# Performance work log

Hardware: AMD Instinct MI355X
Metric: run time of the kernel (lower is better)

Reference implementation:

```python
import jax, jax.numpy as jnp
import numpy as np
from math import sqrt

B, S, D_MODEL, H, DK, DV = 16, 512, 256, 8, 32, 32
EPS = 1e-5


def layer_norm(x, g, b):
    m = jnp.mean(x, axis=-1, keepdims=True)
    v = jnp.mean((x - m) ** 2, axis=-1, keepdims=True)
    return g * (x - m) / jnp.sqrt(v + EPS) + b


def setup_inputs() -> dict:
    key = jax.random.key(0)
    ks = jax.random.split(key, 16)
    inp = {
        "input_Q": jax.random.normal(ks[0], (B, S, D_MODEL), jnp.float32),
        "input_K": jax.random.normal(ks[1], (B, S, D_MODEL), jnp.float32),
        "input_V": jax.random.normal(ks[2], (B, S, D_MODEL), jnp.float32),
        "attn_mask": jax.random.bernoulli(ks[3], 0.1, (B, H, S, S)),
        "matrix": jax.random.uniform(ks[4], (B, S, S), jnp.float32),
        # learned params (stored [in, out], i.e. transpose of torch Linear weight)
        "W_Q": jax.random.normal(ks[5], (D_MODEL, H * DK), jnp.float32) * 0.02,
        "W_K": jax.random.normal(ks[6], (D_MODEL, H * DK), jnp.float32) * 0.02,
        "W_V": jax.random.normal(ks[7], (D_MODEL, H * DV), jnp.float32) * 0.02,
        "W_V2": jax.random.normal(ks[8], (D_MODEL, DV), jnp.float32) * 0.02,
        "W_fc": jax.random.normal(ks[9], (DV * (H + 1), D_MODEL), jnp.float32) * 0.02,
        "ln_g": jnp.ones((D_MODEL,), jnp.float32),
        "ln_b": jnp.zeros((D_MODEL,), jnp.float32),
        "fu_ln_g": jnp.ones((H + 1,), jnp.float32),
        "fu_ln_b": jnp.zeros((H + 1,), jnp.float32),
        "fu_w1": jax.random.normal(ks[10], (H + 1, 6), jnp.float32) * 0.3,
        "fu_b1": jnp.zeros((6,), jnp.float32),
        "fu_w2": jax.random.normal(ks[11], (6, 1), jnp.float32) * 0.3,
        "fu_b2": jnp.zeros((1,), jnp.float32),
    }
    return inp


def reference(input_Q, input_K, input_V, attn_mask, matrix,
              W_Q, W_K, W_V, W_V2, W_fc, ln_g, ln_b,
              fu_ln_g, fu_ln_b, fu_w1, fu_b1, fu_w2, fu_b2):
    b = input_Q.shape[0]
    # project and split heads: [B, H, S, d]
    Q = (input_Q @ W_Q).reshape(b, -1, H, DK).transpose(0, 2, 1, 3)
    K = (input_K @ W_K).reshape(b, -1, H, DK).transpose(0, 2, 1, 3)
    V = (input_V @ W_V).reshape(b, -1, H, DV).transpose(0, 2, 1, 3)
    scores = jnp.einsum('bhqd,bhkd->bhqk', Q, K) / sqrt(DK)
    scores = jnp.where(attn_mask, -1e9, scores)
    attn = jax.nn.softmax(scores, axis=-1)            # [B, H, S, S]
    context = jnp.einsum('bhqk,bhkd->bhqd', attn, V)  # [B, H, S, DV]
    # second context from pairwise matrix
    context2 = matrix @ (input_V @ W_V2)              # [B, S, DV]
    # gated matrix update: concat matrix with attn maps along head axis
    gate_in = jnp.concatenate([matrix[:, None], attn], axis=1)  # [B, H+1, S, S]
    gate_in = gate_in.transpose(0, 3, 2, 1)                     # [B, S, S, H+1]
    g = layer_norm(gate_in, fu_ln_g, fu_ln_b)
    g = jax.nn.relu(g @ fu_w1 + fu_b1)
    g = jax.nn.sigmoid(g @ fu_w2 + fu_b2)[..., 0]               # [B, S, S]
    matrix_out = matrix * g
    # merge heads, concat, project, layernorm
    context = context.transpose(0, 2, 1, 3).reshape(b, -1, H * DV)
    context = jnp.concatenate([context, context2], axis=-1)     # [B, S, DV*(H+1)]
    output = layer_norm(context @ W_fc, ln_g, ln_b)
    return (output, matrix_out)
```

## Files before the change

### kernel.cpp

```cpp
#include <hip/hip_runtime.h>
#include <hip/hip_bf16.h>

#define BB 16
#define SS 512
#define DM 256
#define NH 8

#define OFF_QB    0
#define OFF_KB    1048576
#define OFF_VT    2097152
#define OFF_VP2   3145728
#define OFF_CTXB  3407872
#define OFF_CTX2B 4456448
#define OFF_G     4587520
#define OFF_FLAG  6684672
#define OFF_PM    6684674

#define SCALE 0.17677669529663687f
#define KE2 0.2550348623f

typedef __attribute__((ext_vector_type(8))) short bfrag8;
typedef __attribute__((ext_vector_type(4))) float facc4;

__global__ void mask_or_kernel(const unsigned int* __restrict__ w,
                               unsigned int* __restrict__ acc) {
  __shared__ unsigned int sh[256];
  unsigned int a = 0;
  int base = blockIdx.x * 1024;
  for (int i = threadIdx.x; i < 1024; i += 256) a |= w[base + i];
  sh[threadIdx.x] = a;
  __syncthreads();
  for (int s = 128; s > 0; s >>= 1) {
    if (threadIdx.x < s) sh[threadIdx.x] |= sh[threadIdx.x + s];
    __syncthreads();
  }
  if (threadIdx.x == 0) atomicOr(acc, sh[0]);
}

__global__ __launch_bounds__(256) void mask_pack_kernel(
    const void* __restrict__ mask, unsigned long long* __restrict__ pm,
    const unsigned int* __restrict__ orv) {
  const unsigned int rawor = *orv;
  const int flagv = (rawor <= 1u) ? 0 : ((rawor == 0x3F800000u) ? 2 : 1);
  const int lane = threadIdx.x & 63;
  const int wv = threadIdx.x >> 6;
  const int w0 = (blockIdx.x * 4 + wv) * 32;
  const unsigned char* mb = (const unsigned char*)mask;
  const int* mi = (const int*)mask;
  const float* mf = (const float*)mask;
  unsigned long long myw = 0;
#pragma unroll 4
  for (int i = 0; i < 32; i++) {
    long long idx = (long long)(w0 + i) * 64 + lane;
    bool m;
    if (flagv == 1) m = (mb[idx] != 0);
    else if (flagv == 0) m = (mi[idx] != 0);
    else m = (mf[idx] != 0.f);
    unsigned long long bits = __ballot(m);
    if (lane == i) myw = bits;
  }
  if (lane < 32) pm[w0 + lane] = myw;
}

__global__ __launch_bounds__(256) void gemm_qkv_kernel(
    const float* __restrict__ inQ, const float* __restrict__ inK,
    const float* __restrict__ inV,
    const float* __restrict__ Wq, const float* __restrict__ Wk,
    const float* __restrict__ Wv,
    __hip_bfloat16* __restrict__ Qb, __hip_bfloat16* __restrict__ Kb,
    __hip_bfloat16* __restrict__ Vt) {
  __shared__ __align__(16) __hip_bfloat16 As[64][40];
  __shared__ __align__(16) __hip_bfloat16 Bs[64][40];
  const int tid = threadIdx.x;
  const int bid = blockIdx.x;
  const int matid = bid >> 9;
  const int mblk = (bid & 511) >> 2;
  const int nblk = bid & 3;
  const int m0 = mblk * 64;
  const int n0 = nblk * 64;
  const float* X = (matid == 0) ? inQ : (matid == 1) ? inK : inV;
  const float* W = (matid == 0) ? Wq : (matid == 1) ? Wk : Wv;

  const int lane = tid & 63;
  const int w = tid >> 6;
  const int wm = w & 1, wn = w >> 1;
  const int cl = lane & 15, quad = lane >> 4;
  const int arow = tid >> 2, ak8 = (tid & 3) * 8;
  const int bn = tid & 63, bk8 = (tid >> 6) * 8;

  facc4 acc[2][2];
#pragma unroll
  for (int t = 0; t < 2; t++)
#pragma unroll
    for (int u = 0; u < 2; u++) acc[t][u] = (facc4){0.f, 0.f, 0.f, 0.f};

#pragma unroll 1
  for (int kc = 0; kc < 8; kc++) {
    float4 x0 = *(const float4*)&X[(m0 + arow) * 256 + kc * 32 + ak8];
    float4 x1 = *(const float4*)&X[(m0 + arow) * 256 + kc * 32 + ak8 + 4];
    float wv[8];
#pragma unroll
    for (int j = 0; j < 8; j++) wv[j] = W[(kc * 32 + bk8 + j) * 256 + n0 + bn];
    __syncthreads();
    {
      __hip_bfloat16 ta[8];
      ta[0] = __float2bfloat16(x0.x); ta[1] = __float2bfloat16(x0.y);
      ta[2] = __float2bfloat16(x0.z); ta[3] = __float2bfloat16(x0.w);
      ta[4] = __float2bfloat16(x1.x); ta[5] = __float2bfloat16(x1.y);
      ta[6] = __float2bfloat16(x1.z); ta[7] = __float2bfloat16(x1.w);
      *(uint4*)&As[arow][ak8] = *(uint4*)ta;
      __hip_bfloat16 tb[8];
#pragma unroll
      for (int j = 0; j < 8; j++) tb[j] = __float2bfloat16(wv[j]);
      *(uint4*)&Bs[bn][bk8] = *(uint4*)tb;
    }
    __syncthreads();
    bfrag8 aA[2], bB[2];
#pragma unroll
    for (int t = 0; t < 2; t++)
      aA[t] = *(const bfrag8*)&As[wm * 32 + t * 16 + cl][quad * 8];
#pragma unroll
    for (int u = 0; u < 2; u++)
      bB[u] = *(const bfrag8*)&Bs[wn * 32 + u * 16 + cl][quad * 8];
#pragma unroll
    for (int t = 0; t < 2; t++)
#pragma unroll
      for (int u = 0; u < 2; u++)
        acc[t][u] =
            __builtin_amdgcn_mfma_f32_16x16x32_bf16(aA[t], bB[u], acc[t][u], 0, 0, 0);
  }

  if (matid < 2) {
    __hip_bfloat16* Y = (matid == 0) ? Qb : Kb;
#pragma unroll
    for (int t = 0; t < 2; t++)
#pragma unroll
      for (int u = 0; u < 2; u++)
#pragma unroll
        for (int reg = 0; reg < 4; reg++)
          Y[(m0 + wm * 32 + t * 16 + quad * 4 + reg) * 256 + n0 + wn * 32 +
            u * 16 + cl] = __float2bfloat16(acc[t][u][reg]);
  } else {
#pragma unroll
    for (int t = 0; t < 2; t++)
#pragma unroll
      for (int u = 0; u < 2; u++) {
        int c = n0 + wn * 32 + u * 16 + cl;
        int mg = m0 + wm * 32 + t * 16 + quad * 4;
        int b = mg >> 9, s = mg & 511;
        __hip_bfloat16 pk[4];
#pragma unroll
        for (int reg = 0; reg < 4; reg++)
          pk[reg] = __float2bfloat16(acc[t][u][reg]);
        *(ushort4*)&Vt[(((b << 8) + c) << 9) + s] = *(ushort4*)pk;
      }
  }
}

__global__ __launch_bounds__(256) void vp2_kernel(
    const float* __restrict__ inV, const float* __restrict__ Wv2,
    float* __restrict__ Vp2) {
  __shared__ __align__(16) float xs[16][260];
  const int t = threadIdx.x;
  const int r0 = blockIdx.x * 16;
  for (int e = t; e < 16 * 256; e += 256) {
    int r = e >> 8, i = e & 255;
    xs[r][i] = inV[(r0 + r) * 256 + i];
  }
  __syncthreads();
  const int c2 = t & 31, rr = t >> 5;
  float a0 = 0.f, a1 = 0.f;
  for (int i = 0; i < 256; i += 4) {
    float w0 = Wv2[i * 32 + c2], w1 = Wv2[(i + 1) * 32 + c2];
    float w2 = Wv2[(i + 2) * 32 + c2], w3 = Wv2[(i + 3) * 32 + c2];
    float4 xa = *(const float4*)&xs[rr][i];
    float4 xb = *(const float4*)&xs[rr + 8][i];
    a0 += xa.x * w0 + xa.y * w1 + xa.z * w2 + xa.w * w3;
    a1 += xb.x * w0 + xb.y * w1 + xb.z * w2 + xb.w * w3;
  }
  Vp2[(r0 + rr) * 32 + c2] = a0;
  Vp2[(r0 + rr + 8) * 32 + c2] = a1;
}

__global__ __launch_bounds__(512, 2) void attn_kernel(
    const __hip_bfloat16* __restrict__ Qb, const __hip_bfloat16* __restrict__ Kb,
    const __hip_bfloat16* __restrict__ Vt,
    const unsigned long long* __restrict__ pm,
    const float* __restrict__ matrix,
    const float* __restrict__ fulng, const float* __restrict__ fulnb,
    const float* __restrict__ fuw1, const float* __restrict__ fub1,
    const float* __restrict__ fuw2, const float* __restrict__ fub2,
    __hip_bfloat16* __restrict__ ctxb, __hip_bfloat16* __restrict__ gws) {
  __shared__ __align__(16) __hip_bfloat16 Sb[NH][16][520];
  __shared__ float inv_s[NH][16];
  __shared__ float gp[80];

  const int tid = threadIdx.x;
  const int lane = tid & 63;
  const int h = tid >> 6;
  const int cl = lane & 15, quad = lane >> 4;
  const int b = ((blockIdx.x & 7) << 1) | (blockIdx.x >> 8);
  const int q0 = ((blockIdx.x >> 3) & 31) * 16;

  if (tid < 6) {
    const int j = tid;
    float s1 = 0.f, c1 = fub1[j];
#pragma unroll
    for (int t = 0; t < 9; t++) {
      float w = fuw1[t * 6 + j];
      float gw = fulng[t] * w;
      gp[t * 6 + j] = gw;
      s1 += gw;
      c1 += fulnb[t] * w;
    }
    gp[54 + j] = s1;
    gp[60 + j] = c1;
    gp[66 + j] = fuw2[j];
    if (j == 0) gp[72] = fub2[0];
  }

  const unsigned long long* pmb = pm + (((b * NH + h) << 9) + q0) * 8;

  const bfrag8 aQ =
      *(const bfrag8*)&Qb[(((b << 9) + q0 + cl) << 8) + h * 32 + quad * 8];
  const __hip_bfloat16* KbB = &Kb[((b << 9) << 8) + h * 32 + quad * 8];
  const __hip_bfloat16* VtB = &Vt[(((b << 8) + h * 32) << 9)];

  float l[4] = {0.f, 0.f, 0.f, 0.f};
#pragma unroll 4
  for (int w8 = 0; w8 < 8; w8++) {
    unsigned long long mw[4];
#pragma unroll
    for (int r = 0; r < 4; r++)
      mw[r] = pmb[(quad * 4 + r) * 8 + w8] >> cl;
#pragma unroll
    for (int n4 = 0; n4 < 4; n4++) {
      const int nt = w8 * 4 + n4;
      bfrag8 bK = *(const bfrag8*)&KbB[(nt * 16 + cl) << 8];
      facc4 cc = {0.f, 0.f, 0.f, 0.f};
      cc = __builtin_amdgcn_mfma_f32_16x16x32_bf16(aQ, bK, cc, 0, 0, 0);
#pragma unroll
      for (int r = 0; r < 4; r++) {
        float e = ((mw[r] >> (n4 * 16)) & 1ULL) ? 0.f : exp2f(KE2 * cc[r]);
        l[r] += e;
        Sb[h][quad * 4 + r][nt * 16 + cl] = __float2bfloat16(e);
      }
    }
  }
#pragma unroll
  for (int r = 0; r < 4; r++)
#pragma unroll
    for (int off = 1; off <= 8; off <<= 1) l[r] += __shfl_xor(l[r], off);
  float invl[4];
#pragma unroll
  for (int r = 0; r < 4; r++) invl[r] = 1.f / l[r];
  if (cl == 0) {
#pragma unroll
    for (int r = 0; r < 4; r++) inv_s[h][quad * 4 + r] = invl[r];
  }
  __syncthreads();

  facc4 a0 = {0.f, 0.f, 0.f, 0.f}, a1 = {0.f, 0.f, 0.f, 0.f};
#pragma unroll 8
  for (int ks = 0; ks < 16; ks++) {
    bfrag8 aP = *(const bfrag8*)&Sb[h][cl][ks * 32 + quad * 8];
    bfrag8 b0 = *(const bfrag8*)&VtB[(cl << 9) + ks * 32 + quad * 8];
    bfrag8 b1 = *(const bfrag8*)&VtB[((16 + cl) << 9) + ks * 32 + quad * 8];
    a0 = __builtin_amdgcn_mfma_f32_16x16x32_bf16(aP, b0, a0, 0, 0, 0);
    a1 = __builtin_amdgcn_mfma_f32_16x16x32_bf16(aP, b1, a1, 0, 0, 0);
  }

  {
    const int gq = tid >> 5;
    const int g32 = (tid & 31) * 4;
#pragma unroll 2
    for (int s = 0; s < 4; s++) {
      const int k4 = s * 128 + g32;
      float4 mrow =
          *(const float4*)&matrix[((b << 9) + q0 + gq) * 512 + k4];
      float p[NH][4];
#pragma unroll
      for (int hh = 0; hh < NH; hh++) {
        const float iv = inv_s[hh][gq];
        ushort4 sv = *(const ushort4*)&Sb[hh][gq][k4];
        p[hh][0] = __bfloat162float(*(__hip_bfloat16*)&sv.x) * iv;
        p[hh][1] = __bfloat162float(*(__hip_bfloat16*)&sv.y) * iv;
        p[hh][2] = __bfloat162float(*(__hip_bfloat16*)&sv.z) * iv;
        p[hh][3] = __bfloat162float(*(__hip_bfloat16*)&sv.w) * iv;
      }
      const float mcomp[4] = {mrow.x, mrow.y, mrow.z, mrow.w};
      __hip_bfloat16 gout[4];
#pragma unroll
      for (int i = 0; i < 4; i++) {
        float v[9];
        v[0] = mcomp[i];
#pragma unroll
        for (int t = 0; t < NH; t++) v[1 + t] = p[t][i];
        float s1 = 0.f, s2 = 0.f;
#pragma unroll
        for (int t = 0; t < 9; t++) {
          s1 += v[t];
          s2 += v[t] * v[t];
        }
        float mu = s1 * (1.f / 9.f);
        float var = s2 * (1.f / 9.f) - mu * mu;
        float inv = rsqrtf(var + 1e-5f);
        float o = gp[72];
#pragma unroll
        for (int j = 0; j < 6; j++) {
          float d = 0.f;
#pragma unroll
          for (int t = 0; t < 9; t++) d += v[t] * gp[t * 6 + j];
          float z = inv * (d - mu * gp[54 + j]) + gp[60 + j];
          z = fmaxf(z, 0.f);
          o += z * gp[66 + j];
        }
        gout[i] = __float2bfloat16(1.f / (1.f + __expf(-o)));
      }
      *(ushort4*)&gws[((b << 9) + q0 + gq) * 512 + k4] = *(ushort4*)gout;
    }
  }

#pragma unroll
  for (int r = 0; r < 4; r++) {
    int row = quad * 4 + r;
    ctxb[((b << 9) + q0 + row) * 256 + h * 32 + cl] =
        __float2bfloat16(a0[r] * invl[r]);
    ctxb[((b << 9) + q0 + row) * 256 + h * 32 + 16 + cl] =
        __float2bfloat16(a1[r] * invl[r]);
  }
}

__global__ __launch_bounds__(256) void mout_kernel(
    const float* __restrict__ matrix, const __hip_bfloat16* __restrict__ g,
    float* __restrict__ mout) {
  __shared__ float Gs[64][65];
  const int tid = threadIdx.x;
  const int b = blockIdx.x >> 6;
  const int j0 = ((blockIdx.x >> 3) & 7) * 64;
  const int i0 = (blockIdx.x & 7) * 64;

  {
    int r = tid >> 2, c0 = (tid & 3) * 16;
    const __hip_bfloat16* gpx = g + (((b << 9) + i0 + r) << 9) + j0 + c0;
    ushort us[16];
    *(uint4*)(us) = *(const uint4*)(gpx);
    *(uint4*)(us + 8) = *(const uint4*)(gpx + 8);
#pragma unroll
    for (int k = 0; k < 16; k++) {
      __hip_bfloat16 hv = *(__hip_bfloat16*)&us[k];
      Gs[r][c0 + k] = __bfloat162float(hv);
    }
  }
  __syncthreads();

  {
    int jj = tid >> 2, ic = (tid & 3) * 16;
    const float* mp = matrix + (((b << 9) + j0 + jj) << 9) + i0 + ic;
    float* op = mout + (((b << 9) + j0 + jj) << 9) + i0 + ic;
#pragma unroll
    for (int v4 = 0; v4 < 4; v4++) {
      float4 m = *(const float4*)(mp + v4 * 4);
      float4 o;
      o.x = m.x * Gs[ic + v4 * 4 + 0][jj];
      o.y = m.y * Gs[ic + v4 * 4 + 1][jj];
      o.z = m.z * Gs[ic + v4 * 4 + 2][jj];
      o.w = m.w * Gs[ic + v4 * 4 + 3][jj];
      *(float4*)(op + v4 * 4) = o;
    }
  }
}

__global__ __launch_bounds__(256) void ctx2_kernel(
    const float* __restrict__ matrix, const float* __restrict__ Vp2,
    __hip_bfloat16* __restrict__ ctx2b) {
  __shared__ __align__(16) float Ms[16][128];
  __shared__ __align__(16) float Vs2t[32][132];
  const int t = threadIdx.x;
  const int b = blockIdx.x >> 5;
  const int s0 = (blockIdx.x & 31) * 16;
  const int dv = t & 31, rg = t >> 5;
  float acc0 = 0.f, acc1 = 0.f;
  for (int kc = 0; kc < 4; kc++) {
    __syncthreads();
#pragma unroll
    for (int it = 0; it < 8; it++) {
      int idx = t + it * 256;
      int r = idx >> 7, cc = idx & 127;
      Ms[r][cc] = matrix[((b << 9) + s0 + r) * 512 + kc * 128 + cc];
    }
#pragma unroll
    for (int it = 0; it < 16; it++) {
      int e = t + it * 256;
      int k = e >> 5, dv2 = e & 31;
      Vs2t[dv2][k] = Vp2[((b << 9) + kc * 128 + k) * 32 + dv2];
    }
    __syncthreads();
    for (int k = 0; k < 128; k += 4) {
      float4 vv = *(const float4*)&Vs2t[dv][k];
      float4 m0 = *(const float4*)&Ms[rg][k];
      float4 m1 = *(const float4*)&Ms[rg + 8][k];
      acc0 += m0.x * vv.x + m0.y * vv.y + m0.z * vv.z + m0.w * vv.w;
      acc1 += m1.x * vv.x + m1.y * vv.y + m1.z * vv.z + m1.w * vv.w;
    }
  }
  ctx2b[((b << 9) + s0 + rg) * 32 + dv] = __float2bfloat16(acc0);
  ctx2b[((b << 9) + s0 + rg + 8) * 32 + dv] = __float2bfloat16(acc1);
}

__global__ __launch_bounds__(256) void final_kernel(
    const __hip_bfloat16* __restrict__ ctxb,
    const __hip_bfloat16* __restrict__ ctx2b, const float* __restrict__ Wfc,
    const float* __restrict__ lng, const float* __restrict__ lnb,
    float* __restrict__ out) {
  __shared__ __align__(16) __hip_bfloat16 As[32][40];
  __shared__ __align__(16) __hip_bfloat16 Bs[256][40];
  __shared__ __align__(16) float xs[32][260];
  __shared__ float red2[32][8][2];
  __shared__ float musig[32][2];
  const int tid = threadIdx.x;
  const int m0 = blockIdx.x * 32;
  const int lane = tid & 63, w = tid >> 6;
  const int cl = lane & 15, quad = lane >> 4;
  const int arow = tid >> 3, ak4 = (tid & 7) * 4;

  facc4 acc[2][4];
#pragma unroll
  for (int t = 0; t < 2; t++)
#pragma unroll
    for (int u = 0; u < 4; u++) acc[t][u] = (facc4){0.f, 0.f, 0.f, 0.f};

#pragma unroll 1
  for (int kc = 0; kc < 9; kc++) {
    ushort4 av;
    if (kc < 8)
      av = *(const ushort4*)&ctxb[(m0 + arow) * 256 + kc * 32 + ak4];
    else
      av = *(const ushort4*)&ctx2b[(m0 + arow) * 32 + ak4];
    float wv[32];
#pragma unroll
    for (int j = 0; j < 32; j++) wv[j] = Wfc[(kc * 32 + j) * 256 + tid];
    __syncthreads();
    *(ushort4*)&As[arow][ak4] = av;
    {
      __hip_bfloat16 tw[32];
#pragma unroll
      for (int j = 0; j < 32; j++) tw[j] = __float2bfloat16(wv[j]);
#pragma unroll
      for (int g = 0; g < 4; g++) *(uint4*)&Bs[tid][g * 8] = *(uint4*)&tw[g * 8];
    }
    __syncthreads();
    bfrag8 aA[2], bB[4];
#pragma unroll
    for (int t = 0; t < 2; t++)
      aA[t] = *(const bfrag8*)&As[t * 16 + cl][quad * 8];
#pragma unroll
    for (int u = 0; u < 4; u++)
      bB[u] = *(const bfrag8*)&Bs[w * 64 + u * 16 + cl][quad * 8];
#pragma unroll
    for (int t = 0; t < 2; t++)
#pragma unroll
      for (int u = 0; u < 4; u++)
        acc[t][u] =
            __builtin_amdgcn_mfma_f32_16x16x32_bf16(aA[t], bB[u], acc[t][u], 0, 0, 0);
  }

#pragma unroll
  for (int t = 0; t < 2; t++)
#pragma unroll
    for (int u = 0; u < 4; u++)
#pragma unroll
      for (int reg = 0; reg < 4; reg++)
        xs[t * 16 + quad * 4 + reg][w * 64 + u * 16 + cl] = acc[t][u][reg];
  __syncthreads();

  {
    int r = tid >> 3, c0 = (tid & 7) * 32;
    float s1 = 0.f, s2 = 0.f;
    for (int j = 0; j < 32; j += 4) {
      float4 v = *(const float4*)&xs[r][c0 + j];
      s1 += v.x + v.y + v.z + v.w;
      s2 += v.x * v.x + v.y * v.y + v.z * v.z + v.w * v.w;
    }
    red2[r][tid & 7][0] = s1;
    red2[r][tid & 7][1] = s2;
  }
  __syncthreads();
  if (tid < 32) {
    float s1 = 0.f, s2 = 0.f;
#pragma unroll
    for (int j = 0; j < 8; j++) {
      s1 += red2[tid][j][0];
      s2 += red2[tid][j][1];
    }
    float mu = s1 * (1.f / 256.f);
    float var = s2 * (1.f / 256.f) - mu * mu;
    musig[tid][0] = mu;
    musig[tid][1] = rsqrtf(var + 1e-5f);
  }
  __syncthreads();
  {
    float gt = lng[tid], bt = lnb[tid];
#pragma unroll 4
    for (int r = 0; r < 32; r++)
      out[(m0 + r) * 256 + tid] =
          gt * (xs[r][tid] - musig[r][0]) * musig[r][1] + bt;
  }
}

extern "C" void kernel_launch(void* const* d_in, const int* in_sizes, int n_in,
                              void* d_out, int out_size, void* d_ws,
                              size_t ws_size, hipStream_t stream) {
  const float* inQ = (const float*)d_in[0];
  const float* inK = (const float*)d_in[1];
  const float* inV = (const float*)d_in[2];
  const void* mask = d_in[3];
  const float* matrix = (const float*)d_in[4];
  const float* Wq = (const float*)d_in[5];
  const float* Wk = (const float*)d_in[6];
  const float* Wv = (const float*)d_in[7];
  const float* Wv2 = (const float*)d_in[8];
  const float* Wfc = (const float*)d_in[9];
  const float* lng = (const float*)d_in[10];
  const float* lnb = (const float*)d_in[11];
  const float* fulng = (const float*)d_in[12];
  const float* fulnb = (const float*)d_in[13];
  const float* fuw1 = (const float*)d_in[14];
  const float* fub1 = (const float*)d_in[15];
  const float* fuw2 = (const float*)d_in[16];
  const float* fub2 = (const float*)d_in[17];

  float* ws = (float*)d_ws;
  __hip_bfloat16* Qb = (__hip_bfloat16*)(ws + OFF_QB);
  __hip_bfloat16* Kb = (__hip_bfloat16*)(ws + OFF_KB);
  __hip_bfloat16* Vt = (__hip_bfloat16*)(ws + OFF_VT);
  float* Vp2 = ws + OFF_VP2;
  __hip_bfloat16* ctxb = (__hip_bfloat16*)(ws + OFF_CTXB);
  __hip_bfloat16* ctx2b = (__hip_bfloat16*)(ws + OFF_CTX2B);
  __hip_bfloat16* gws = (__hip_bfloat16*)(ws + OFF_G);
  unsigned int* flag = (unsigned int*)(ws + OFF_FLAG);
  unsigned long long* pmask = (unsigned long long*)(ws + OFF_PM);

  float* out = (float*)d_out;
  float* mout = out + BB * SS * DM;

  hipMemsetAsync(flag, 0, 4, stream);
  mask_or_kernel<<<64, 256, 0, stream>>>((const unsigned int*)mask, flag);
  mask_pack_kernel<<<4096, 256, 0, stream>>>(mask, pmask, flag);
  gemm_qkv_kernel<<<1536, 256, 0, stream>>>(inQ, inK, inV, Wq, Wk, Wv, Qb, Kb,
                                            Vt);
  vp2_kernel<<<512, 256, 0, stream>>>(inV, Wv2, Vp2);
  attn_kernel<<<512, 512, 0, stream>>>(Qb, Kb, Vt, pmask, matrix, fulng, fulnb,
                                       fuw1, fub1, fuw2, fub2, ctxb, gws);
  mout_kernel<<<BB * 64, 256, 0, stream>>>(matrix, gws, mout);
  ctx2_kernel<<<512, 256, 0, stream>>>(matrix, Vp2, ctx2b);
  final_kernel<<<256, 256, 0, stream>>>(ctxb, ctx2b, Wfc, lng, lnb, out);
}
```

Measured before the change: 396.2 us.

## Merge independent kernels and pick mask packing path from input byte size

Merges the QKV projection GEMM with the V2 projection, and the matrix-gating output with the context2 matmul, into single launches that dispatch on block index. When the mask buffer is 4 bytes per element, the memset and flag-detection kernel are skipped and a dedicated 32-bit packing kernel runs instead. Unroll factors in the attention kernel loops are also reduced, likely to ease register pressure. This cuts launch count and lets independent work share the GPU, at the cost of heterogeneous blocks inside one grid.

```diff
diff --git a/kernel.cpp b/kernel.cpp
--- a/kernel.cpp
+++ b/kernel.cpp
@@ -62,124 +62,139 @@
   if (lane < 32) pm[w0 + lane] = myw;
 }
 
-__global__ __launch_bounds__(256) void gemm_qkv_kernel(
+__global__ __launch_bounds__(256) void mask_pack4_kernel(
+    const unsigned int* __restrict__ mask, unsigned long long* __restrict__ pm) {
+  const int lane = threadIdx.x & 63;
+  const int wv = threadIdx.x >> 6;
+  const int w0 = (blockIdx.x * 4 + wv) * 32;
+  unsigned long long myw = 0;
+#pragma unroll 4
+  for (int i = 0; i < 32; i++) {
+    unsigned int v = mask[(long long)(w0 + i) * 64 + lane];
+    unsigned long long bits = __ballot(v != 0u);
+    if (lane == i) myw = bits;
+  }
+  if (lane < 32) pm[w0 + lane] = myw;
+}
+
+__global__ __launch_bounds__(256) void gemm_qkv_vp2_kernel(
     const float* __restrict__ inQ, const float* __restrict__ inK,
     const float* __restrict__ inV,
     const float* __restrict__ Wq, const float* __restrict__ Wk,
-    const float* __restrict__ Wv,
+    const float* __restrict__ Wv, const float* __restrict__ Wv2,
     __hip_bfloat16* __restrict__ Qb, __hip_bfloat16* __restrict__ Kb,
-    __hip_bfloat16* __restrict__ Vt) {
-  __shared__ __align__(16) __hip_bfloat16 As[64][40];
-  __shared__ __align__(16) __hip_bfloat16 Bs[64][40];
+    __hip_bfloat16* __restrict__ Vt, float* __restrict__ Vp2) {
+  __shared__ __align__(16) char smem[16640];
   const int tid = threadIdx.x;
-  const int bid = blockIdx.x;
-  const int matid = bid >> 9;
-  const int mblk = (bid & 511) >> 2;
-  const int nblk = bid & 3;
-  const int m0 = mblk * 64;
-  const int n0 = nblk * 64;
-  const float* X = (matid == 0) ? inQ : (matid == 1) ? inK : inV;
-  const float* W = (matid == 0) ? Wq : (matid == 1) ? Wk : Wv;
-
-  const int lane = tid & 63;
-  const int w = tid >> 6;
-  const int wm = w & 1, wn = w >> 1;
-  const int cl = lane & 15, quad = lane >> 4;
-  const int arow = tid >> 2, ak8 = (tid & 3) * 8;
-  const int bn = tid & 63, bk8 = (tid >> 6) * 8;
-
-  facc4 acc[2][2];
-#pragma unroll
-  for (int t = 0; t < 2; t++)
-#pragma unroll
-    for (int u = 0; u < 2; u++) acc[t][u] = (facc4){0.f, 0.f, 0.f, 0.f};
+
+  if (blockIdx.x < 1536) {
+    auto As = reinterpret_cast<__hip_bfloat16(*)[40]>(smem);
+    auto Bs = reinterpret_cast<__hip_bfloat16(*)[40]>(smem + 5120);
+    const int bid = blockIdx.x;
+    const int matid = bid >> 9;
+    const int mblk = (bid & 511) >> 2;
+    const int nblk = bid & 3;
+    const int m0 = mblk * 64;
+    const int n0 = nblk * 64;
+    const float* X = (matid == 0) ? inQ : (matid == 1) ? inK : inV;
+    const float* W = (matid == 0) ? Wq : (matid == 1) ? Wk : Wv;
+
+    const int lane = tid & 63;
+    const int w = tid >> 6;
+    const int wm = w & 1, wn = w >> 1;
+    const int cl = lane & 15, quad = lane >> 4;
+    const int arow = tid >> 2, ak8 = (tid & 3) * 8;
+    const int bn = tid & 63, bk8 = (tid >> 6) * 8;
+
+    facc4 acc[2][2];
+#pragma unroll
+    for (int t = 0; t < 2; t++)
+#pragma unroll
+      for (int u = 0; u < 2; u++) acc[t][u] = (facc4){0.f, 0.f, 0.f, 0.f};
 
 #pragma unroll 1
-  for (int kc = 0; kc < 8; kc++) {
-    float4 x0 = *(const float4*)&X[(m0 + arow) * 256 + kc * 32 + ak8];
-    float4 x1 = *(const float4*)&X[(m0 + arow) * 256 + kc * 32 + ak8 + 4];
-    float wv[8];
-#pragma unroll
-    for (int j = 0; j < 8; j++) wv[j] = W[(kc * 32 + bk8 + j) * 256 + n0 + bn];
+    for (int kc = 0; kc < 8; kc++) {
+      float4 x0 = *(const float4*)&X[(m0 + arow) * 256 + kc * 32 + ak8];
+      float4 x1 = *(const float4*)&X[(m0 + arow) * 256 + kc * 32 + ak8 + 4];
+      float wv[8];
+#pragma unroll
+      for (int j = 0; j < 8; j++)
+        wv[j] = W[(kc * 32 + bk8 + j) * 256 + n0 + bn];
+      __syncthreads();
+      {
+        __hip_bfloat16 ta[8];
+        ta[0] = __float2bfloat16(x0.x); ta[1] = __float2bfloat16(x0.y);
+        ta[2] = __float2bfloat16(x0.z); ta[3] = __float2bfloat16(x0.w);
+        ta[4] = __float2bfloat16(x1.x); ta[5] = __float2bfloat16(x1.y);
+        ta[6] = __float2bfloat16(x1.z); ta[7] = __float2bfloat16(x1.w);
+        *(uint4*)&As[arow][ak8] = *(uint4*)ta;
+        __hip_bfloat16 tb[8];
+#pragma unroll
+        for (int j = 0; j < 8; j++) tb[j] = __float2bfloat16(wv[j]);
+        *(uint4*)&Bs[bn][bk8] = *(uint4*)tb;
+      }
+      __syncthreads();
+      bfrag8 aA[2], bB[2];
+#pragma unroll
+      for (int t = 0; t < 2; t++)
+        aA[t] = *(const bfrag8*)&As[wm * 32 + t * 16 + cl][quad * 8];
+#pragma unroll
+      for (int u = 0; u < 2; u++)
+        bB[u] = *(const bfrag8*)&Bs[wn * 32 + u * 16 + cl][quad * 8];
+#pragma unroll
+      for (int t = 0; t < 2; t++)
+#pragma unroll
+        for (int u = 0; u < 2; u++)
+          acc[t][u] = __builtin_amdgcn_mfma_f32_16x16x32_bf16(aA[t], bB[u],
+                                                             acc[t][u], 0, 0, 0);
+    }
+
+    if (matid < 2) {
+      __hip_bfloat16* Y = (matid == 0) ? Qb : Kb;
+#pragma unroll
+      for (int t = 0; t < 2; t++)
+#pragma unroll
+        for (int u = 0; u < 2; u++)
+#pragma unroll
+          for (int reg = 0; reg < 4; reg++)
+            Y[(m0 + wm * 32 + t * 16 + quad * 4 + reg) * 256 + n0 + wn * 32 +
+              u * 16 + cl] = __float2bfloat16(acc[t][u][reg]);
+    } else {
+#pragma unroll
+      for (int t = 0; t < 2; t++)
+#pragma unroll
+        for (int u = 0; u < 2; u++) {
+          int c = n0 + wn * 32 + u * 16 + cl;
+          int mg = m0 + wm * 32 + t * 16 + quad * 4;
+          int b = mg >> 9, s = mg & 511;
+          __hip_bfloat16 pk[4];
+#pragma unroll
+          for (int reg = 0; reg < 4; reg++)
+            pk[reg] = __float2bfloat16(acc[t][u][reg]);
+          *(ushort4*)&Vt[(((b << 8) + c) << 9) + s] = *(ushort4*)pk;
+        }
+    }
+  } else {
+    auto xs = reinterpret_cast<float(*)[260]>(smem);
+    const int r0 = (blockIdx.x - 1536) * 16;
+    for (int e = tid; e < 16 * 256; e += 256) {
+      int r = e >> 8, i = e & 255;
+      xs[r][i] = inV[(r0 + r) * 256 + i];
+    }
     __syncthreads();
-    {
-      __hip_bfloat16 ta[8];
-      ta[0] = __float2bfloat16(x0.x); ta[1] = __float2bfloat16(x0.y);
-      ta[2] = __float2bfloat16(x0.z); ta[3] = __float2bfloat16(x0.w);
-      ta[4] = __float2bfloat16(x1.x); ta[5] = __float2bfloat16(x1.y);
-      ta[6] = __float2bfloat16(x1.z); ta[7] = __float2bfloat16(x1.w);
-      *(uint4*)&As[arow][ak8] = *(uint4*)ta;
-      __hip_bfloat16 tb[8];
-#pragma unroll
-      for (int j = 0; j < 8; j++) tb[j] = __float2bfloat16(wv[j]);
-      *(uint4*)&Bs[bn][bk8] = *(uint4*)tb;
-    }
-    __syncthreads();
-    bfrag8 aA[2], bB[2];
-#pragma unroll
-    for (int t = 0; t < 2; t++)
-      aA[t] = *(const bfrag8*)&As[wm * 32 + t * 16 + cl][quad * 8];
-#pragma unroll
-    for (int u = 0; u < 2; u++)
-      bB[u] = *(const bfrag8*)&Bs[wn * 32 + u * 16 + cl][quad * 8];
-#pragma unroll
-    for (int t = 0; t < 2; t++)
-#pragma unroll
-      for (int u = 0; u < 2; u++)
-        acc[t][u] =
-            __builtin_amdgcn_mfma_f32_16x16x32_bf16(aA[t], bB[u], acc[t][u], 0, 0, 0);
-  }
-
-  if (matid < 2) {
-    __hip_bfloat16* Y = (matid == 0) ? Qb : Kb;
-#pragma unroll
-    for (int t = 0; t < 2; t++)
-#pragma unroll
-      for (int u = 0; u < 2; u++)
-#pragma unroll
-        for (int reg = 0; reg < 4; reg++)
-          Y[(m0 + wm * 32 + t * 16 + quad * 4 + reg) * 256 + n0 + wn * 32 +
-            u * 16 + cl] = __float2bfloat16(acc[t][u][reg]);
-  } else {
-#pragma unroll
-    for (int t = 0; t < 2; t++)
-#pragma unroll
-      for (int u = 0; u < 2; u++) {
-        int c = n0 + wn * 32 + u * 16 + cl;
-        int mg = m0 + wm * 32 + t * 16 + quad * 4;
-        int b = mg >> 9, s = mg & 511;
-        __hip_bfloat16 pk[4];
-#pragma unroll
-        for (int reg = 0; reg < 4; reg++)
-          pk[reg] = __float2bfloat16(acc[t][u][reg]);
-        *(ushort4*)&Vt[(((b << 8) + c) << 9) + s] = *(ushort4*)pk;
-      }
-  }
-}
-
-__global__ __launch_bounds__(256) void vp2_kernel(
-    const float* __restrict__ inV, const float* __restrict__ Wv2,
-    float* __restrict__ Vp2) {
-  __shared__ __align__(16) float xs[16][260];
-  const int t = threadIdx.x;
-  const int r0 = blockIdx.x * 16;
-  for (int e = t; e < 16 * 256; e += 256) {
-    int r = e >> 8, i = e & 255;
-    xs[r][i] = inV[(r0 + r) * 256 + i];
-  }
-  __syncthreads();
-  const int c2 = t & 31, rr = t >> 5;
-  float a0 = 0.f, a1 = 0.f;
-  for (int i = 0; i < 256; i += 4) {
-    float w0 = Wv2[i * 32 + c2], w1 = Wv2[(i + 1) * 32 + c2];
-    float w2 = Wv2[(i + 2) * 32 + c2], w3 = Wv2[(i + 3) * 32 + c2];
-    float4 xa = *(const float4*)&xs[rr][i];
-    float4 xb = *(const float4*)&xs[rr + 8][i];
-    a0 += xa.x * w0 + xa.y * w1 + xa.z * w2 + xa.w * w3;
-    a1 += xb.x * w0 + xb.y * w1 + xb.z * w2 + xb.w * w3;
-  }
-  Vp2[(r0 + rr) * 32 + c2] = a0;
-  Vp2[(r0 + rr + 8) * 32 + c2] = a1;
+    const int c2 = tid & 31, rr = tid >> 5;
+    float a0 = 0.f, a1 = 0.f;
+    for (int i = 0; i < 256; i += 4) {
+      float w0 = Wv2[i * 32 + c2], w1 = Wv2[(i + 1) * 32 + c2];
+      float w2 = Wv2[(i + 2) * 32 + c2], w3 = Wv2[(i + 3) * 32 + c2];
+      float4 xa = *(const float4*)&xs[rr][i];
+      float4 xb = *(const float4*)&xs[rr + 8][i];
+      a0 += xa.x * w0 + xa.y * w1 + xa.z * w2 + xa.w * w3;
+      a1 += xb.x * w0 + xb.y * w1 + xb.z * w2 + xb.w * w3;
+    }
+    Vp2[(r0 + rr) * 32 + c2] = a0;
+    Vp2[(r0 + rr + 8) * 32 + c2] = a1;
+  }
 }
 
 __global__ __launch_bounds__(512, 2) void attn_kernel(
@@ -227,7 +242,7 @@
   const __hip_bfloat16* VtB = &Vt[(((b << 8) + h * 32) << 9)];
 
   float l[4] = {0.f, 0.f, 0.f, 0.f};
-#pragma unroll 4
+#pragma unroll 2
   for (int w8 = 0; w8 < 8; w8++) {
     unsigned long long mw[4];
 #pragma unroll
@@ -261,7 +276,7 @@
   __syncthreads();
 
   facc4 a0 = {0.f, 0.f, 0.f, 0.f}, a1 = {0.f, 0.f, 0.f, 0.f};
-#pragma unroll 8
+#pragma unroll 4
   for (int ks = 0; ks < 16; ks++) {
     bfrag8 aP = *(const bfrag8*)&Sb[h][cl][ks * 32 + quad * 8];
     bfrag8 b0 = *(const bfrag8*)&VtB[(cl << 9) + ks * 32 + quad * 8];
@@ -273,7 +288,7 @@
   {
     const int gq = tid >> 5;
     const int g32 = (tid & 31) * 4;
-#pragma unroll 2
+#pragma unroll 1
     for (int s = 0; s < 4; s++) {
       const int k4 = s * 128 + g32;
       float4 mrow =
@@ -331,81 +346,82 @@
   }
 }
 
-__global__ __launch_bounds__(256) void mout_kernel(
+__global__ __launch_bounds__(256) void mout_ctx2_kernel(
     const float* __restrict__ matrix, const __hip_bfloat16* __restrict__ g,
-    float* __restrict__ mout) {
-  __shared__ float Gs[64][65];
+    float* __restrict__ mout, const float* __restrict__ Vp2,
+    __hip_bfloat16* __restrict__ ctx2b) {
+  __shared__ __align__(16) char smem[25088];
   const int tid = threadIdx.x;
-  const int b = blockIdx.x >> 6;
-  const int j0 = ((blockIdx.x >> 3) & 7) * 64;
-  const int i0 = (blockIdx.x & 7) * 64;
-
-  {
-    int r = tid >> 2, c0 = (tid & 3) * 16;
-    const __hip_bfloat16* gpx = g + (((b << 9) + i0 + r) << 9) + j0 + c0;
-    ushort us[16];
-    *(uint4*)(us) = *(const uint4*)(gpx);
-    *(uint4*)(us + 8) = *(const uint4*)(gpx + 8);
-#pragma unroll
-    for (int k = 0; k < 16; k++) {
-      __hip_bfloat16 hv = *(__hip_bfloat16*)&us[k];
-      Gs[r][c0 + k] = __bfloat162float(hv);
-    }
-  }
-  __syncthreads();
-
-  {
-    int jj = tid >> 2, ic = (tid & 3) * 16;
-    const float* mp = matrix + (((b << 9) + j0 + jj) << 9) + i0 + ic;
-    float* op = mout + (((b << 9) + j0 + jj) << 9) + i0 + ic;
-#pragma unroll
-    for (int v4 = 0; v4 < 4; v4++) {
-      float4 m = *(const float4*)(mp + v4 * 4);
-      float4 o;
-      o.x = m.x * Gs[ic + v4 * 4 + 0][jj];
-      o.y = m.y * Gs[ic + v4 * 4 + 1][jj];
-      o.z = m.z * Gs[ic + v4 * 4 + 2][jj];
-      o.w = m.w * Gs[ic + v4 * 4 + 3][jj];
-      *(float4*)(op + v4 * 4) = o;
-    }
-  }
-}
-
-__global__ __launch_bounds__(256) void ctx2_kernel(
-    const float* __restrict__ matrix, const float* __restrict__ Vp2,
-    __hip_bfloat16* __restrict__ ctx2b) {
-  __shared__ __align__(16) float Ms[16][128];
-  __shared__ __align__(16) float Vs2t[32][132];
-  const int t = threadIdx.x;
-  const int b = blockIdx.x >> 5;
-  const int s0 = (blockIdx.x & 31) * 16;
-  const int dv = t & 31, rg = t >> 5;
-  float acc0 = 0.f, acc1 = 0.f;
-  for (int kc = 0; kc < 4; kc++) {
+
+  if (blockIdx.x < 1024) {
+    auto Gs = reinterpret_cast<float(*)[65]>(smem);
+    const int b = blockIdx.x >> 6;
+    const int j0 = ((blockIdx.x >> 3) & 7) * 64;
+    const int i0 = (blockIdx.x & 7) * 64;
+
+    {
+      int r = tid >> 2, c0 = (tid & 3) * 16;
+      const __hip_bfloat16* gpx = g + (((b << 9) + i0 + r) << 9) + j0 + c0;
+      ushort us[16];
+      *(uint4*)(us) = *(const uint4*)(gpx);
+      *(uint4*)(us + 8) = *(const uint4*)(gpx + 8);
+#pragma unroll
+      for (int k = 0; k < 16; k++) {
+        __hip_bfloat16 hv = *(__hip_bfloat16*)&us[k];
+        Gs[r][c0 + k] = __bfloat162float(hv);
+      }
+    }
     __syncthreads();
-#pragma unroll
-    for (int it = 0; it < 8; it++) {
-      int idx = t + it * 256;
-      int r = idx >> 7, cc = idx & 127;
-      Ms[r][cc] = matrix[((b << 9) + s0 + r) * 512 + kc * 128 + cc];
-    }
-#pragma unroll
-    for (int it = 0; it < 16; it++) {
-      int e = t + it * 256;
-      int k = e >> 5, dv2 = e & 31;
-      Vs2t[dv2][k] = Vp2[((b << 9) + kc * 128 + k) * 32 + dv2];
-    }
-    __syncthreads();
-    for (int k = 0; k < 128; k += 4) {
-      float4 vv = *(const float4*)&Vs2t[dv][k];
-      float4 m0 = *(const float4*)&Ms[rg][k];
-      float4 m1 = *(const float4*)&Ms[rg + 8][k];
-      acc0 += m0.x * vv.x + m0.y * vv.y + m0.z * vv.z + m0.w * vv.w;
-      acc1 += m1.x * vv.x + m1.y * vv.y + m1.z * vv.z + m1.w * vv.w;
-    }
-  }
-  ctx2b[((b << 9) + s0 + rg) * 32 + dv] = __float2bfloat16(acc0);
-  ctx2b[((b << 9) + s0 + rg + 8) * 32 + dv] = __float2bfloat16(acc1);
+
+    {
+      int jj = tid >> 2, ic = (tid & 3) * 16;
+      const float* mp = matrix + (((b << 9) + j0 + jj) << 9) + i0 + ic;
+      float* op = mout + (((b << 9) + j0 + jj) << 9) + i0 + ic;
+#pragma unroll
+      for (int v4 = 0; v4 < 4; v4++) {
+        float4 m = *(const float4*)(mp + v4 * 4);
+        float4 o;
+        o.x = m.x * Gs[ic + v4 * 4 + 0][jj];
+        o.y = m.y * Gs[ic + v4 * 4 + 1][jj];
+        o.z = m.z * Gs[ic + v4 * 4 + 2][jj];
+        o.w = m.w * Gs[ic + v4 * 4 + 3][jj];
+        *(float4*)(op + v4 * 4) = o;
+      }
+    }
+  } else {
+    auto Ms = reinterpret_cast<float(*)[128]>(smem);
+    auto Vs2t = reinterpret_cast<float(*)[132]>(smem + 8192);
+    const int cid = blockIdx.x - 1024;
+    const int b = cid >> 5;
+    const int s0 = (cid & 31) * 16;
+    const int dv = tid & 31, rg = tid >> 5;
+    float acc0 = 0.f, acc1 = 0.f;
+    for (int kc = 0; kc < 4; kc++) {
+      __syncthreads();
+#pragma unroll
+      for (int it = 0; it < 8; it++) {
+        int idx = tid + it * 256;
+        int r = idx >> 7, cc = idx & 127;
+        Ms[r][cc] = matrix[((b << 9) + s0 + r) * 512 + kc * 128 + cc];
+      }
+#pragma unroll
+      for (int it = 0; it < 16; it++) {
+        int e = tid + it * 256;
+        int k = e >> 5, dv2 = e & 31;
+        Vs2t[dv2][k] = Vp2[((b << 9) + kc * 128 + k) * 32 + dv2];
+      }
+      __syncthreads();
+      for (int k = 0; k < 128; k += 4) {
+        float4 vv = *(const float4*)&Vs2t[dv][k];
+        float4 m0 = *(const float4*)&Ms[rg][k];
+        float4 m1 = *(const float4*)&Ms[rg + 8][k];
+        acc0 += m0.x * vv.x + m0.y * vv.y + m0.z * vv.z + m0.w * vv.w;
+        acc1 += m1.x * vv.x + m1.y * vv.y + m1.z * vv.z + m1.w * vv.w;
+      }
+    }
+    ctx2b[((b << 9) + s0 + rg) * 32 + dv] = __float2bfloat16(acc0);
+    ctx2b[((b << 9) + s0 + rg + 8) * 32 + dv] = __float2bfloat16(acc1);
+  }
 }
 
 __global__ __launch_bounds__(256) void final_kernel(
@@ -544,15 +560,19 @@
   float* out = (float*)d_out;
   float* mout = out + BB * SS * DM;
 
-  hipMemsetAsync(flag, 0, 4, stream);
-  mask_or_kernel<<<64, 256, 0, stream>>>((const unsigned int*)mask, flag);
-  mask_pack_kernel<<<4096, 256, 0, stream>>>(mask, pmask, flag);
-  gemm_qkv_kernel<<<1536, 256, 0, stream>>>(inQ, inK, inV, Wq, Wk, Wv, Qb, Kb,
-                                            Vt);
-  vp2_kernel<<<512, 256, 0, stream>>>(inV, Wv2, Vp2);
+  const long long MASKN = (long long)BB * NH * SS * SS;
+  if (in_sizes[3] == (int)(MASKN * 4)) {
+    mask_pack4_kernel<<<4096, 256, 0, stream>>>((const unsigned int*)mask,
+                                                pmask);
+  } else {
+    hipMemsetAsync(flag, 0, 4, stream);
+    mask_or_kernel<<<64, 256, 0, stream>>>((const unsigned int*)mask, flag);
+    mask_pack_kernel<<<4096, 256, 0, stream>>>(mask, pmask, flag);
+  }
+  gemm_qkv_vp2_kernel<<<2048, 256, 0, stream>>>(inQ, inK, inV, Wq, Wk, Wv, Wv2,
+                                                Qb, Kb, Vt, Vp2);
   attn_kernel<<<512, 512, 0, stream>>>(Qb, Kb, Vt, pmask, matrix, fulng, fulnb,
                                        fuw1, fub1, fuw2, fub2, ctxb, gws);
-  mout_kernel<<<BB * 64, 256, 0, stream>>>(matrix, gws, mout);
-  ctx2_kernel<<<512, 256, 0, stream>>>(matrix, Vp2, ctx2b);
+  mout_ctx2_kernel<<<1536, 256, 0, stream>>>(matrix, gws, mout, Vp2, ctx2b);
   final_kernel<<<256, 256, 0, stream>>>(ctxb, ctx2b, Wfc, lng, lnb, out);
 }
```

Measured after the change: 381.8 us. -3.7%, faster.
